# Optimization experiments

Measured on AMD Instinct MI355X. Metric: run time of the kernel, lower is better.

Reference implementation:

```python
import jax, jax.numpy as jnp
import numpy as np

D = 1024
F = 256
EPS = 1e-5


def layer_norm(x, g, b):
    mu = jnp.mean(x, axis=-1, keepdims=True)
    var = jnp.mean((x - mu) ** 2, axis=-1, keepdims=True)
    return (x - mu) * jax.lax.rsqrt(var + EPS) * g + b


def setup_inputs() -> dict:
    key = jax.random.key(0)
    ks = jax.random.split(key, 8)
    B, S = 4, 4096
    return {
        "bottom_up_input": jax.random.normal(ks[0], (B, S, D), dtype=jnp.float32),
        "top_down_prediction": jax.random.normal(ks[1], (B, S, D), dtype=jnp.float32),
        "W_spec": jax.random.normal(ks[2], (2 * F, D), dtype=jnp.float32) * 0.02,
        "log_decay": jnp.linspace(-3.0, -0.001, F, dtype=jnp.float32),
        "frequencies": jax.random.normal(ks[3], (F,), dtype=jnp.float32) * 0.1,
        "W_from": jax.random.normal(ks[4], (D, 2 * F), dtype=jnp.float32) * 0.02,
        "ln1_g": jnp.ones((D,), jnp.float32),
        "ln1_b": jnp.zeros((D,), jnp.float32),
        "W1": jax.random.normal(ks[5], (D, D), dtype=jnp.float32) * 0.02,
        "b1": jnp.zeros((D,), jnp.float32),
        "W2": jax.random.normal(ks[6], (D, D), dtype=jnp.float32) * 0.02,
        "b2": jnp.zeros((D,), jnp.float32),
        "ln2_g": jnp.ones((D,), jnp.float32),
        "ln2_b": jnp.zeros((D,), jnp.float32),
        "error_weight": jnp.asarray(0.1, jnp.float32),
    }


def spectral_conv(x, W_spec, log_decay, frequencies, W_from, ln1_g, ln1_b):
    # x: [B,S,D]
    x = layer_norm(x, ln1_g, ln1_b)
    B, S, _ = x.shape
    spectral = jnp.einsum('bsd,fd->bsf', x, W_spec)  # [B,S,2F]
    u = jax.lax.complex(spectral[..., :F], spectral[..., F:])  # [B,S,F] complex
    decay = jax.nn.sigmoid(log_decay)
    omega = jnp.tanh(frequencies) * 0.1  # dt = 1.0
    rot = jax.lax.complex(jnp.cos(omega), jnp.sin(omega))  # [F]
    A = (decay * rot).astype(jnp.complex64)  # [F]
    # kernel[t] = A^t * rot, built with cumprod as in the original
    ones = jnp.ones((1, F), dtype=A.dtype)
    A_seq = jnp.broadcast_to(A[None, :], (S - 1, F))
    powers = jnp.cumprod(jnp.concatenate([ones, A_seq], axis=0), axis=0)  # [S,F]
    kernel = (powers * rot[None, :])[None]  # [1,S,F]
    n_fft = 2 * S
    U_f = jnp.fft.fft(u, n=n_fft, axis=1)
    K_f = jnp.fft.fft(kernel, n=n_fft, axis=1)
    y = jnp.fft.ifft(U_f * K_f, n=n_fft, axis=1)[:, :S, :]  # [B,S,F]
    spectral_out = jnp.concatenate([y.real, y.imag], axis=-1)  # [B,S,2F]
    return jnp.einsum('bsf,df->bsd', spectral_out, W_from)


def reference(bottom_up_input, top_down_prediction, W_spec, log_decay, frequencies,
              W_from, ln1_g, ln1_b, W1, b1, W2, b2, ln2_g, ln2_b, error_weight):
    bu_repr = spectral_conv(bottom_up_input, W_spec, log_decay, frequencies,
                            W_from, ln1_g, ln1_b)
    error = jnp.clip(bu_repr - top_down_prediction, -1.0, 1.0)
    corrected = bu_repr - jax.nn.sigmoid(error_weight) * error
    prediction_error = jnp.clip(jnp.mean(error ** 2), 0.0, 1.0)
    h = jax.nn.gelu(jnp.einsum('bsd,ed->bse', corrected, W1) + b1, approximate=False)
    h = jnp.einsum('bsd,ed->bse', h, W2) + b2
    next_prediction = layer_norm(h, ln2_g, ln2_b)
    return corrected, next_prediction, prediction_error
```

## Files before the change

kernel.cpp:

```cpp
#include <hip/hip_runtime.h>
#include <math.h>

#define Dn 1024
#define Fn 256
#define Sn 4096
#define Bn 4
#define Mn (Bn*Sn)
#define CHn 16
#define NCn (Sn/CHn)

typedef __bf16 bf16x8 __attribute__((ext_vector_type(8)));
typedef float  f32x4  __attribute__((ext_vector_type(4)));

__device__ inline unsigned short f2bf(float f) {
  unsigned int u = __float_as_uint(f);
  u += 0x7fffu + ((u >> 16) & 1u);
  return (unsigned short)(u >> 16);
}
__device__ inline float bf2f(unsigned short s) {
  return __uint_as_float(((unsigned int)s) << 16);
}

__device__ inline void async16(const void* g, void* l) {
  __builtin_amdgcn_global_load_lds(
      (__attribute__((address_space(1))) void*)(g),
      (__attribute__((address_space(3))) void*)(l), 16, 0, 0);
}

#define WAITVM(n) __builtin_amdgcn_s_waitcnt(0xF70 | (n))
#define BARRIER() asm volatile("s_barrier" ::: "memory")

__global__ __launch_bounds__(256) void ln1_conv(
    const float* __restrict__ x, const float* __restrict__ g,
    const float* __restrict__ b, unsigned short* __restrict__ out,
    const float* __restrict__ wspec, const float* __restrict__ wfrom,
    const float* __restrict__ w1, const float* __restrict__ w2,
    unsigned short* __restrict__ o_spec, unsigned short* __restrict__ o_from,
    unsigned short* __restrict__ o_w1, unsigned short* __restrict__ o_w2) {
  int tid = threadIdx.x;
  int gid = blockIdx.x * 256 + tid;
  o_w1[gid] = f2bf(w1[gid]);
  o_w2[gid] = f2bf(w2[gid]);
  if (gid < 524288) {
    o_spec[gid] = f2bf(wspec[gid]);
    o_from[gid] = f2bf(wfrom[gid]);
  }

  int wid = tid >> 6, lane = tid & 63;
  int row = blockIdx.x * 4 + wid;
  const float4* xr = (const float4*)x + (size_t)row * 256;
  float4 v[4];
  float s = 0.0f, ss = 0.0f;
  #pragma unroll
  for (int k = 0; k < 4; k++) {
    v[k] = xr[lane + 64 * k];
    s  += v[k].x + v[k].y + v[k].z + v[k].w;
    ss += v[k].x * v[k].x + v[k].y * v[k].y + v[k].z * v[k].z + v[k].w * v[k].w;
  }
  #pragma unroll
  for (int o = 32; o; o >>= 1) {
    s  += __shfl_xor(s, o);
    ss += __shfl_xor(ss, o);
  }
  float mu  = s * (1.0f / Dn);
  float var = ss * (1.0f / Dn) - mu * mu;
  float rs  = rsqrtf(var + 1e-5f);
  ushort4* orow = (ushort4*)out + (size_t)row * 256;
  #pragma unroll
  for (int k = 0; k < 4; k++) {
    float4 gv = ((const float4*)g)[lane + 64 * k];
    float4 bv = ((const float4*)b)[lane + 64 * k];
    ushort4 w;
    w.x = f2bf((v[k].x - mu) * rs * gv.x + bv.x);
    w.y = f2bf((v[k].y - mu) * rs * gv.y + bv.y);
    w.z = f2bf((v[k].z - mu) * rs * gv.z + bv.z);
    w.w = f2bf((v[k].w - mu) * rs * gv.w + bv.w);
    orow[lane + 64 * k] = w;
  }
}

__global__ __launch_bounds__(256) void ln2_err(
    const unsigned short* __restrict__ h, const float* __restrict__ g,
    const float* __restrict__ b, float* __restrict__ out,
    const float* __restrict__ errAcc, float* __restrict__ outErr) {
  int tid = threadIdx.x;
  if (blockIdx.x == 0 && tid == 0) {
    float m = errAcc[0] * (1.0f / 16777216.0f);
    outErr[0] = fminf(fmaxf(m, 0.0f), 1.0f);
  }
  int wid = tid >> 6, lane = tid & 63;
  int row = blockIdx.x * 4 + wid;
  const ushort4* xr = (const ushort4*)h + (size_t)row * 256;
  float4 v[4];
  float s = 0.0f, ss = 0.0f;
  #pragma unroll
  for (int k = 0; k < 4; k++) {
    ushort4 u = xr[lane + 64 * k];
    v[k].x = bf2f(u.x); v[k].y = bf2f(u.y); v[k].z = bf2f(u.z); v[k].w = bf2f(u.w);
    s  += v[k].x + v[k].y + v[k].z + v[k].w;
    ss += v[k].x * v[k].x + v[k].y * v[k].y + v[k].z * v[k].z + v[k].w * v[k].w;
  }
  #pragma unroll
  for (int o = 32; o; o >>= 1) {
    s  += __shfl_xor(s, o);
    ss += __shfl_xor(ss, o);
  }
  float mu  = s * (1.0f / Dn);
  float var = ss * (1.0f / Dn) - mu * mu;
  float rs  = rsqrtf(var + 1e-5f);
  float4* orow = (float4*)out + (size_t)row * 256;
  #pragma unroll
  for (int k = 0; k < 4; k++) {
    float4 gv = ((const float4*)g)[lane + 64 * k];
    float4 bv = ((const float4*)b)[lane + 64 * k];
    float4 w;
    w.x = (v[k].x - mu) * rs * gv.x + bv.x;
    w.y = (v[k].y - mu) * rs * gv.y + bv.y;
    w.z = (v[k].z - mu) * rs * gv.z + bv.z;
    w.w = (v[k].w - mu) * rs * gv.w + bv.w;
    orow[lane + 64 * k] = w;
  }
}

template <int MODE>
__global__ __launch_bounds__(256, 4) void gemm_bt(
    const unsigned short* __restrict__ A, const unsigned short* __restrict__ Bw,
    int K, int N,
    float* __restrict__ outF, unsigned short* __restrict__ outH,
    const float* __restrict__ td, const float* __restrict__ bias,
    const float* __restrict__ ew, float* __restrict__ errAcc) {
  __shared__ unsigned short As[2 * 4096];
  __shared__ unsigned short Bs[2 * 4096];
  __shared__ float red[4];

  int tid = threadIdx.x;
  int wid = tid >> 6, lane = tid & 63;
  int wm = wid >> 1, wn = wid & 1;
  int quad = lane >> 4, l16 = lane & 15;

  int g = blockIdx.x + gridDim.x * blockIdx.y;
  int nbn = gridDim.x;
  int gh = g >> 3;
  int bn = gh % nbn;
  int bm = (g & 7) + (gh / nbn) * 8;

  int r_lo = lane >> 2;
  int c8   = (lane & 3) * 8;

  const unsigned short* Abase = A + (size_t)bm * 128 * K;
  const unsigned short* Bbase = Bw + (size_t)bn * 128 * K;

  f32x4 acc[4][4] = {};

  const int T = K >> 5;
  auto issue = [&](int t, int stg) {
    int k0 = t << 5;
    #pragma unroll
    for (int s = 0; s < 2; ++s) {
      int chunk = s * 4 + wid;
      int r = chunk * 16 + r_lo;
      async16(Abase + (size_t)r * K + k0 + c8, As + stg * 4096 + chunk * 512);
      async16(Bbase + (size_t)r * K + k0 + c8, Bs + stg * 4096 + chunk * 512);
    }
  };

  issue(0, 0);

  for (int k = 0; k < T; ++k) {
    WAITVM(0);
    BARRIER();
    if (k + 1 < T) issue(k + 1, (k + 1) & 1);

    const unsigned short* Ab = As + (k & 1) * 4096;
    const unsigned short* Bb = Bs + (k & 1) * 4096;
    bf16x8 af[4], bf[4];
    #pragma unroll
    for (int i = 0; i < 4; i++)
      af[i] = *(const bf16x8*)(Ab + (wm * 64 + i * 16 + l16) * 32 + quad * 8);
    #pragma unroll
    for (int j = 0; j < 4; j++)
      bf[j] = *(const bf16x8*)(Bb + (wn * 64 + j * 16 + l16) * 32 + quad * 8);
    #pragma unroll
    for (int i = 0; i < 4; i++)
      #pragma unroll
      for (int j = 0; j < 4; j++)
        acc[i][j] = __builtin_amdgcn_mfma_f32_16x16x32_bf16(af[i], bf[j], acc[i][j], 0, 0, 0);
  }

  float esum = 0.0f;
  float sigw = 0.0f;
  if (MODE == 1) sigw = 1.0f / (1.0f + expf(-ew[0]));

  #pragma unroll
  for (int i = 0; i < 4; i++) {
    int row_base = bm * 128 + wm * 64 + i * 16 + quad * 4;
    #pragma unroll
    for (int j = 0; j < 4; j++) {
      int col = bn * 128 + wn * 64 + j * 16 + l16;
      #pragma unroll
      for (int r = 0; r < 4; r++) {
        size_t idx = (size_t)(row_base + r) * N + col;
        float v = acc[i][j][r];
        if (MODE == 0) {
          outH[idx] = f2bf(v);
        } else if (MODE == 1) {
          float e = v - td[idx];
          e = fminf(fmaxf(e, -1.0f), 1.0f);
          float corr = v - sigw * e;
          outF[idx] = corr;
          outH[idx] = f2bf(corr);
          esum += e * e;
        } else if (MODE == 2) {
          float h = v + bias[col];
          float gel = 0.5f * h * (1.0f + erff(h * 0.70710678118654752f));
          outH[idx] = f2bf(gel);
        } else if (MODE == 3) {
          outF[idx] = v + bias[col];
        } else {
          outH[idx] = f2bf(v + bias[col]);
        }
      }
    }
  }

  if (MODE == 1) {
    #pragma unroll
    for (int o = 32; o; o >>= 1) esum += __shfl_down(esum, o);
    if (lane == 0) red[wid] = esum;
    __syncthreads();
    if (tid == 0) atomicAdd(errAcc, red[0] + red[1] + red[2] + red[3]);
  }
}

template <int MODE, int NBN>
__global__ __launch_bounds__(512, 2) void gemm256(
    const unsigned short* __restrict__ A, const unsigned short* __restrict__ Bw,
    int K,
    float* __restrict__ outF, unsigned short* __restrict__ outH,
    const float* __restrict__ td, const float* __restrict__ bias,
    const float* __restrict__ ew, float* __restrict__ errAcc) {
  __shared__ unsigned short As[2 * 16384];
  __shared__ unsigned short Bs[2 * 16384];
  __shared__ float red[8];

  const int tid = threadIdx.x;
  const int w = tid >> 6, l = tid & 63;
  const int wm = w >> 2, wn = w & 3;
  const int quad = l >> 4, l16 = l & 15;
  const int sw = l16 & 7;
  const int N = NBN * 256;

  int g = blockIdx.x;
  int gh = g >> 3;
  int bn = gh % NBN;
  int bm = (g & 7) + (gh / NBN) * 8;

  const int r8 = w * 8 + (l >> 3);
  const int gcol = ((l & 7) ^ (l >> 3)) * 8;
  const unsigned short* Ag = A + (size_t)(bm * 256 + r8) * K + gcol;
  const unsigned short* Bg = Bw + (size_t)(bn * 256 + r8) * K + gcol;

  auto stage = [&](int t, int c) {
    const int k0 = t << 6;
    #pragma unroll
    for (int i = 0; i < 4; i++) {
      async16(Ag + (size_t)(i * 64) * K + k0, As + c * 16384 + i * 4096 + w * 512);
      async16(Bg + (size_t)(i * 64) * K + k0, Bs + c * 16384 + i * 4096 + w * 512);
    }
  };

  f32x4 acc[8][4] = {};
  const int NT = K >> 6;

  stage(0, 0);
  stage(1, 1);
  WAITVM(8);
  BARRIER();

  for (int t = 0; t < NT; ++t) {
    const int c = t & 1;
    const unsigned short* Ab = As + c * 16384;
    const unsigned short* Bb = Bs + c * 16384;
    bf16x8 af[8], bfr[4];

    #pragma unroll
    for (int m = 0; m < 8; m++)
      af[m] = *(const bf16x8*)(Ab + (wm * 128 + m * 16 + l16) * 64 + ((quad ^ sw) << 3));
    #pragma unroll
    for (int n = 0; n < 4; n++)
      bfr[n] = *(const bf16x8*)(Bb + (wn * 64 + n * 16 + l16) * 64 + ((quad ^ sw) << 3));
    BARRIER();
    __builtin_amdgcn_s_setprio(1);
    #pragma unroll
    for (int m = 0; m < 8; m++) {
      acc[m][0] = __builtin_amdgcn_mfma_f32_16x16x32_bf16(af[m], bfr[0], acc[m][0], 0, 0, 0);
      acc[m][1] = __builtin_amdgcn_mfma_f32_16x16x32_bf16(af[m], bfr[1], acc[m][1], 0, 0, 0);
    }
    __builtin_amdgcn_s_setprio(0);
    BARRIER();

    __builtin_amdgcn_s_setprio(1);
    #pragma unroll
    for (int m = 0; m < 8; m++) {
      acc[m][2] = __builtin_amdgcn_mfma_f32_16x16x32_bf16(af[m], bfr[2], acc[m][2], 0, 0, 0);
      acc[m][3] = __builtin_amdgcn_mfma_f32_16x16x32_bf16(af[m], bfr[3], acc[m][3], 0, 0, 0);
    }
    __builtin_amdgcn_s_setprio(0);
    BARRIER();

    #pragma unroll
    for (int m = 0; m < 8; m++)
      af[m] = *(const bf16x8*)(Ab + (wm * 128 + m * 16 + l16) * 64 + (((4 + quad) ^ sw) << 3));
    #pragma unroll
    for (int n = 0; n < 4; n++)
      bfr[n] = *(const bf16x8*)(Bb + (wn * 64 + n * 16 + l16) * 64 + (((4 + quad) ^ sw) << 3));
    BARRIER();
    __builtin_amdgcn_s_setprio(1);
    #pragma unroll
    for (int m = 0; m < 8; m++) {
      acc[m][0] = __builtin_amdgcn_mfma_f32_16x16x32_bf16(af[m], bfr[0], acc[m][0], 0, 0, 0);
      acc[m][1] = __builtin_amdgcn_mfma_f32_16x16x32_bf16(af[m], bfr[1], acc[m][1], 0, 0, 0);
    }
    __builtin_amdgcn_s_setprio(0);
    BARRIER();

    if (t + 2 < NT) { stage(t + 2, c); WAITVM(8); }
    else            { WAITVM(0); }
    BARRIER();
    __builtin_amdgcn_s_setprio(1);
    #pragma unroll
    for (int m = 0; m < 8; m++) {
      acc[m][2] = __builtin_amdgcn_mfma_f32_16x16x32_bf16(af[m], bfr[2], acc[m][2], 0, 0, 0);
      acc[m][3] = __builtin_amdgcn_mfma_f32_16x16x32_bf16(af[m], bfr[3], acc[m][3], 0, 0, 0);
    }
    __builtin_amdgcn_s_setprio(0);
    BARRIER();
  }

  float esum = 0.0f;
  float sigw = 0.0f;
  if (MODE == 1) sigw = 1.0f / (1.0f + expf(-ew[0]));

  #pragma unroll
  for (int m = 0; m < 8; m++) {
    int row_base = bm * 256 + wm * 128 + m * 16 + quad * 4;
    #pragma unroll
    for (int n = 0; n < 4; n++) {
      int col = bn * 256 + wn * 64 + n * 16 + l16;
      #pragma unroll
      for (int r = 0; r < 4; r++) {
        size_t idx = (size_t)(row_base + r) * N + col;
        float v = acc[m][n][r];
        if (MODE == 0) {
          outH[idx] = f2bf(v);
        } else if (MODE == 1) {
          float e = v - td[idx];
          e = fminf(fmaxf(e, -1.0f), 1.0f);
          float corr = v - sigw * e;
          outF[idx] = corr;
          outH[idx] = f2bf(corr);
          esum += e * e;
        } else if (MODE == 2) {
          float h = v + bias[col];
          float gel = 0.5f * h * (1.0f + erff(h * 0.70710678118654752f));
          outH[idx] = f2bf(gel);
        } else if (MODE == 3) {
          outF[idx] = v + bias[col];
        } else {
          outH[idx] = f2bf(v + bias[col]);
        }
      }
    }
  }

  if (MODE == 1) {
    #pragma unroll
    for (int o = 32; o; o >>= 1) esum += __shfl_down(esum, o);
    if (l == 0) red[w] = esum;
    __syncthreads();
    if (tid == 0) {
      float s = 0.0f;
      #pragma unroll
      for (int i = 0; i < 8; i++) s += red[i];
      atomicAdd(errAcc, s);
    }
  }
}

__global__ __launch_bounds__(256) void scan_partial(
    const unsigned short* __restrict__ spec, const float* __restrict__ log_decay,
    const float* __restrict__ freq, float2* __restrict__ chunkfin) {
  int tid = threadIdx.x, wid = tid >> 6, lane = tid & 63;
  int chunk = blockIdx.x * 4 + wid;
  int b = chunk >> 8, c = chunk & (NCn - 1);
  int f0 = lane * 4;
  float Are[4], Aim[4];
  #pragma unroll
  for (int k = 0; k < 4; k++) {
    float dec = 1.0f / (1.0f + expf(-log_decay[f0 + k]));
    float om  = tanhf(freq[f0 + k]) * 0.1f;
    Are[k] = dec * cosf(om); Aim[k] = dec * sinf(om);
  }
  const unsigned short* u = spec + ((size_t)b * Sn + (size_t)c * CHn) * 512;
  float sre[4] = {0, 0, 0, 0}, sim[4] = {0, 0, 0, 0};
  for (int t = 0; t < CHn; t++) {
    ushort4 ur = *(const ushort4*)(u + (size_t)t * 512 + f0);
    ushort4 ui = *(const ushort4*)(u + (size_t)t * 512 + 256 + f0);
    float urf[4] = {bf2f(ur.x), bf2f(ur.y), bf2f(ur.z), bf2f(ur.w)};
    float uif[4] = {bf2f(ui.x), bf2f(ui.y), bf2f(ui.z), bf2f(ui.w)};
    #pragma unroll
    for (int k = 0; k < 4; k++) {
      float nre = Are[k] * sre[k] - Aim[k] * sim[k] + urf[k];
      float nim = Are[k] * sim[k] + Aim[k] * sre[k] + uif[k];
      sre[k] = nre; sim[k] = nim;
    }
  }
  float2* cf = chunkfin + (size_t)chunk * 256 + f0;
  #pragma unroll
  for (int k = 0; k < 4; k++) cf[k] = make_float2(sre[k], sim[k]);
}

__global__ __launch_bounds__(256) void scan_cf(
    const unsigned short* __restrict__ spec, const float* __restrict__ log_decay,
    const float* __restrict__ freq, const float2* __restrict__ chunkfin,
    unsigned short* __restrict__ outH) {
  int tid = threadIdx.x, wid = tid >> 6, lane = tid & 63;
  int chunk = blockIdx.x * 4 + wid;
  int b = chunk >> 8, c = chunk & (NCn - 1);
  int f0 = lane * 4;
  float Are[4], Aim[4], Rre[4], Rim[4], Pre[4], Pim[4];
  #pragma unroll
  for (int k = 0; k < 4; k++) {
    float dec = 1.0f / (1.0f + expf(-log_decay[f0 + k]));
    float om  = tanhf(freq[f0 + k]) * 0.1f;
    Rre[k] = cosf(om); Rim[k] = sinf(om);
    Are[k] = dec * Rre[k]; Aim[k] = dec * Rim[k];
    float pre = Are[k], pim = Aim[k];
    #pragma unroll
    for (int i = 0; i < 4; i++) {
      float nr = pre * pre - pim * pim;
      float ni = 2.0f * pre * pim;
      pre = nr; pim = ni;
    }
    Pre[k] = pre; Pim[k] = pim;
  }
  float sre[4] = {0, 0, 0, 0}, sim[4] = {0, 0, 0, 0};
  const float2* cfb = chunkfin + (size_t)b * NCn * 256;
  for (int j = 0; j < c; j++) {
    #pragma unroll
    for (int k = 0; k < 4; k++) {
      float2 cf = cfb[(size_t)j * 256 + f0 + k];
      float nre = Pre[k] * sre[k] - Pim[k] * sim[k] + cf.x;
      float nim = Pre[k] * sim[k] + Pim[k] * sre[k] + cf.y;
      sre[k] = nre; sim[k] = nim;
    }
  }
  const unsigned short* u = spec + ((size_t)b * Sn + (size_t)c * CHn) * 512;
  unsigned short* o = outH + ((size_t)b * Sn + (size_t)c * CHn) * 512;
  for (int t = 0; t < CHn; t++) {
    ushort4 ur = *(const ushort4*)(u + (size_t)t * 512 + f0);
    ushort4 ui = *(const ushort4*)(u + (size_t)t * 512 + 256 + f0);
    float urf[4] = {bf2f(ur.x), bf2f(ur.y), bf2f(ur.z), bf2f(ur.w)};
    float uif[4] = {bf2f(ui.x), bf2f(ui.y), bf2f(ui.z), bf2f(ui.w)};
    ushort4 wr, wi;
    unsigned short* wrp = &wr.x;
    unsigned short* wip = &wi.x;
    #pragma unroll
    for (int k = 0; k < 4; k++) {
      float nre = Are[k] * sre[k] - Aim[k] * sim[k] + urf[k];
      float nim = Are[k] * sim[k] + Aim[k] * sre[k] + uif[k];
      sre[k] = nre; sim[k] = nim;
      wrp[k] = f2bf(Rre[k] * sre[k] - Rim[k] * sim[k]);
      wip[k] = f2bf(Rre[k] * sim[k] + Rim[k] * sre[k]);
    }
    *(ushort4*)(o + (size_t)t * 512 + f0) = wr;
    *(ushort4*)(o + (size_t)t * 512 + 256 + f0) = wi;
  }
}

extern "C" void kernel_launch(void* const* d_in, const int* in_sizes, int n_in,
                              void* d_out, int out_size, void* d_ws, size_t ws_size,
                              hipStream_t stream) {
  (void)in_sizes; (void)n_in; (void)out_size; (void)ws_size;
  const float* x     = (const float*)d_in[0];
  const float* td    = (const float*)d_in[1];
  const float* wspec = (const float*)d_in[2];
  const float* logd  = (const float*)d_in[3];
  const float* freq  = (const float*)d_in[4];
  const float* wfrom = (const float*)d_in[5];
  const float* g1    = (const float*)d_in[6];
  const float* b1ln  = (const float*)d_in[7];
  const float* W1    = (const float*)d_in[8];
  const float* b1    = (const float*)d_in[9];
  const float* W2    = (const float*)d_in[10];
  const float* b2    = (const float*)d_in[11];
  const float* g2    = (const float*)d_in[12];
  const float* b2ln  = (const float*)d_in[13];
  const float* ew    = (const float*)d_in[14];

  char* ws = (char*)d_ws;
  size_t off = 0;
  float* errAcc = (float*)(ws + off);              off += 256;
  unsigned short* wspec_h = (unsigned short*)(ws + off); off += (size_t)512 * 1024 * 2;
  unsigned short* wfrom_h = (unsigned short*)(ws + off); off += (size_t)1024 * 512 * 2;
  unsigned short* w1_h    = (unsigned short*)(ws + off); off += (size_t)1024 * 1024 * 2;
  unsigned short* w2_h    = (unsigned short*)(ws + off); off += (size_t)1024 * 1024 * 2;
  unsigned short* xn_h   = (unsigned short*)(ws + off);
  unsigned short* corr_h = (unsigned short*)(ws + off);
  unsigned short* h2_h   = (unsigned short*)(ws + off); off += (size_t)Mn * 1024 * 2;
  unsigned short* spec  = (unsigned short*)(ws + off);
  unsigned short* h1_h  = (unsigned short*)(ws + off);  off += (size_t)Mn * 1024 * 2;
  unsigned short* so_h = (unsigned short*)(ws + off);  off += (size_t)Mn * 512 * 2;
  float2* chunkfin = (float2*)(ws + off);              off += (size_t)Bn * NCn * 256 * 8;

  float* outCorr = (float*)d_out;
  float* outNP   = outCorr + (size_t)Mn * 1024;
  float* outErr  = outNP + (size_t)Mn * 1024;

  hipMemsetAsync(errAcc, 0, 4, stream);
  ln1_conv<<<4096, 256, 0, stream>>>(x, g1, b1ln, xn_h,
                                     wspec, wfrom, W1, W2,
                                     wspec_h, wfrom_h, w1_h, w2_h);
  gemm_bt<0><<<dim3(512 / 128, Mn / 128), 256, 0, stream>>>(
      xn_h, wspec_h, 1024, 512, nullptr, spec, nullptr, nullptr, nullptr, nullptr);
  scan_partial<<<256, 256, 0, stream>>>(spec, logd, freq, chunkfin);
  scan_cf<<<256, 256, 0, stream>>>(spec, logd, freq, chunkfin, so_h);
  gemm_bt<1><<<dim3(1024 / 128, Mn / 128), 256, 0, stream>>>(
      so_h, wfrom_h, 512, 1024, outCorr, corr_h, td, nullptr, ew, errAcc);
  gemm256<2, 4><<<256, 512, 0, stream>>>(
      corr_h, w1_h, 1024, nullptr, h1_h, nullptr, b1, nullptr, nullptr);
  gemm256<4, 4><<<256, 512, 0, stream>>>(
      h1_h, w2_h, 1024, nullptr, h2_h, nullptr, b2, nullptr, nullptr);
  ln2_err<<<4096, 256, 0, stream>>>(h2_h, g2, b2ln, outNP, errAcc, outErr);
}
```

Baseline: 533.6 us.

## Replace serial chunk-carry loop with parallel Hillis-Steele scan over chunks

```diff
diff --git a/kernel.cpp b/kernel.cpp
--- a/kernel.cpp
+++ b/kernel.cpp
@@ -6,7 +6,7 @@
 #define Sn 4096
 #define Bn 4
 #define Mn (Bn*Sn)
-#define CHn 16
+#define CHn 8
 #define NCn (Sn/CHn)
 
 typedef __bf16 bf16x8 __attribute__((ext_vector_type(8)));
@@ -392,7 +392,7 @@
     const float* __restrict__ freq, float2* __restrict__ chunkfin) {
   int tid = threadIdx.x, wid = tid >> 6, lane = tid & 63;
   int chunk = blockIdx.x * 4 + wid;
-  int b = chunk >> 8, c = chunk & (NCn - 1);
+  int b = chunk >> 9, c = chunk & (NCn - 1);
   int f0 = lane * 4;
   float Are[4], Aim[4];
   #pragma unroll
@@ -403,6 +403,7 @@
   }
   const unsigned short* u = spec + ((size_t)b * Sn + (size_t)c * CHn) * 512;
   float sre[4] = {0, 0, 0, 0}, sim[4] = {0, 0, 0, 0};
+  #pragma unroll
   for (int t = 0; t < CHn; t++) {
     ushort4 ur = *(const ushort4*)(u + (size_t)t * 512 + f0);
     ushort4 ui = *(const ushort4*)(u + (size_t)t * 512 + 256 + f0);
@@ -415,48 +416,66 @@
       sre[k] = nre; sim[k] = nim;
     }
   }
-  float2* cf = chunkfin + (size_t)chunk * 256 + f0;
-  #pragma unroll
-  for (int k = 0; k < 4; k++) cf[k] = make_float2(sre[k], sim[k]);
-}
-
-__global__ __launch_bounds__(256) void scan_cf(
+  #pragma unroll
+  for (int k = 0; k < 4; k++)
+    chunkfin[((size_t)(b * 256 + f0 + k)) * NCn + c] = make_float2(sre[k], sim[k]);
+}
+
+__global__ __launch_bounds__(512) void scan_carry(
+    const float* __restrict__ log_decay, const float* __restrict__ freq,
+    const float2* __restrict__ chunkfin, float2* __restrict__ carries) {
+  __shared__ float2 buf[NCn];
+  int bf = blockIdx.x;
+  int f = bf & 255;
+  int c = threadIdx.x;
+  float dec = 1.0f / (1.0f + expf(-log_decay[f]));
+  float om  = tanhf(freq[f]) * 0.1f;
+  float Mre = dec * cosf(om), Mim = dec * sinf(om);
+  #pragma unroll
+  for (int i = 0; i < 3; i++) {
+    float nr = Mre * Mre - Mim * Mim;
+    float ni = 2.0f * Mre * Mim;
+    Mre = nr; Mim = ni;
+  }
+  float2 v = chunkfin[(size_t)bf * NCn + c];
+  buf[c] = v;
+  __syncthreads();
+  for (int s = 1; s < NCn; s <<= 1) {
+    float2 w = (c >= s) ? buf[c - s] : make_float2(0.0f, 0.0f);
+    __syncthreads();
+    v.x += Mre * w.x - Mim * w.y;
+    v.y += Mre * w.y + Mim * w.x;
+    buf[c] = v;
+    __syncthreads();
+    float nr = Mre * Mre - Mim * Mim;
+    float ni = 2.0f * Mre * Mim;
+    Mre = nr; Mim = ni;
+  }
+  float2 e = (c == 0) ? make_float2(0.0f, 0.0f) : buf[c - 1];
+  carries[(size_t)bf * NCn + c] = e;
+}
+
+__global__ __launch_bounds__(256) void scan_final(
     const unsigned short* __restrict__ spec, const float* __restrict__ log_decay,
-    const float* __restrict__ freq, const float2* __restrict__ chunkfin,
+    const float* __restrict__ freq, const float2* __restrict__ carries,
     unsigned short* __restrict__ outH) {
   int tid = threadIdx.x, wid = tid >> 6, lane = tid & 63;
   int chunk = blockIdx.x * 4 + wid;
-  int b = chunk >> 8, c = chunk & (NCn - 1);
+  int b = chunk >> 9, c = chunk & (NCn - 1);
   int f0 = lane * 4;
-  float Are[4], Aim[4], Rre[4], Rim[4], Pre[4], Pim[4];
+  float Are[4], Aim[4], Rre[4], Rim[4], sre[4], sim[4];
   #pragma unroll
   for (int k = 0; k < 4; k++) {
     float dec = 1.0f / (1.0f + expf(-log_decay[f0 + k]));
     float om  = tanhf(freq[f0 + k]) * 0.1f;
     Rre[k] = cosf(om); Rim[k] = sinf(om);
     Are[k] = dec * Rre[k]; Aim[k] = dec * Rim[k];
-    float pre = Are[k], pim = Aim[k];
-    #pragma unroll
-    for (int i = 0; i < 4; i++) {
-      float nr = pre * pre - pim * pim;
-      float ni = 2.0f * pre * pim;
-      pre = nr; pim = ni;
-    }
-    Pre[k] = pre; Pim[k] = pim;
-  }
-  float sre[4] = {0, 0, 0, 0}, sim[4] = {0, 0, 0, 0};
-  const float2* cfb = chunkfin + (size_t)b * NCn * 256;
-  for (int j = 0; j < c; j++) {
-    #pragma unroll
-    for (int k = 0; k < 4; k++) {
-      float2 cf = cfb[(size_t)j * 256 + f0 + k];
-      float nre = Pre[k] * sre[k] - Pim[k] * sim[k] + cf.x;
-      float nim = Pre[k] * sim[k] + Pim[k] * sre[k] + cf.y;
-      sre[k] = nre; sim[k] = nim;
-    }
+    float2 s0 = carries[((size_t)(b * 256 + f0 + k)) * NCn + c];
+    sre[k] = s0.x; sim[k] = s0.y;
   }
   const unsigned short* u = spec + ((size_t)b * Sn + (size_t)c * CHn) * 512;
   unsigned short* o = outH + ((size_t)b * Sn + (size_t)c * CHn) * 512;
+  #pragma unroll
   for (int t = 0; t < CHn; t++) {
     ushort4 ur = *(const ushort4*)(u + (size_t)t * 512 + f0);
     ushort4 ui = *(const ushort4*)(u + (size_t)t * 512 + 256 + f0);
@@ -511,7 +530,8 @@
   unsigned short* spec  = (unsigned short*)(ws + off);
   unsigned short* h1_h  = (unsigned short*)(ws + off);  off += (size_t)Mn * 1024 * 2;
   unsigned short* so_h = (unsigned short*)(ws + off);  off += (size_t)Mn * 512 * 2;
-  float2* chunkfin = (float2*)(ws + off);              off += (size_t)Bn * NCn * 256 * 8;
+  float2* chunkfin = (float2*)(ws + off);              off += (size_t)Bn * 256 * NCn * 8;
+  float2* carries  = (float2*)(ws + off);              off += (size_t)Bn * 256 * NCn * 8;
 
   float* outCorr = (float*)d_out;
   float* outNP   = outCorr + (size_t)Mn * 1024;
@@ -523,8 +543,9 @@
                                      wspec_h, wfrom_h, w1_h, w2_h);
   gemm_bt<0><<<dim3(512 / 128, Mn / 128), 256, 0, stream>>>(
       xn_h, wspec_h, 1024, 512, nullptr, spec, nullptr, nullptr, nullptr, nullptr);
-  scan_partial<<<256, 256, 0, stream>>>(spec, logd, freq, chunkfin);
-  scan_cf<<<256, 256, 0, stream>>>(spec, logd, freq, chunkfin, so_h);
+  scan_partial<<<512, 256, 0, stream>>>(spec, logd, freq, chunkfin);
+  scan_carry<<<1024, 512, 0, stream>>>(logd, freq, chunkfin, carries);
+  scan_final<<<512, 256, 0, stream>>>(spec, logd, freq, carries, so_h);
   gemm_bt<1><<<dim3(1024 / 128, Mn / 128), 256, 0, stream>>>(
       so_h, wfrom_h, 512, 1024, outCorr, corr_h, td, nullptr, ew, errAcc);
   gemm256<2, 4><<<256, 512, 0, stream>>>(
```

Result: faster. 469.4 us (-12.0%).
